# Kernel tuning notes

Hardware: AMD Instinct MI355X
Metric: run time of the kernel (lower is better)

The kernel has to match this reference:

```python
import jax, jax.numpy as jnp
import numpy as np

B, N, RESC, LAT, UNIT = 8, 32, 256.0, 1536, 512
CHS = [64, 64, 128, 256, 512, 512]
HS = [128, 64, 32, 16, 8, 1]


def _align(feat, P):
    # torch F.grid_sample(feat, 2*P.unsqueeze(-2)/RESC - 1, 'bilinear', 'border', align_corners=False).squeeze(-1)
    # feat: [B,C,H,W], P: [B,M,2] (x,y) pixel coords in [0,RESC); returns [B,C,M]
    Bn, C, H, W = feat.shape
    gx = 2.0 * P[..., 0] / RESC - 1.0
    gy = 2.0 * P[..., 1] / RESC - 1.0
    # align_corners=False unnormalize, then border clamp
    x = jnp.clip(((gx + 1.0) * W - 1.0) * 0.5, 0.0, W - 1.0)
    y = jnp.clip(((gy + 1.0) * H - 1.0) * 0.5, 0.0, H - 1.0)
    x0 = jnp.floor(x); y0 = jnp.floor(y)
    wx = (x - x0)[:, None, :]; wy = (y - y0)[:, None, :]
    x0i = x0.astype(jnp.int32); y0i = y0.astype(jnp.int32)
    x1i = jnp.minimum(x0i + 1, W - 1); y1i = jnp.minimum(y0i + 1, H - 1)
    flat = feat.reshape(Bn, C, H * W)
    def gat(yi, xi):
        return jnp.take_along_axis(flat, (yi * W + xi)[:, None, :], axis=2)  # [B,C,M]
    v00 = gat(y0i, x0i); v01 = gat(y0i, x1i); v10 = gat(y1i, x0i); v11 = gat(y1i, x1i)
    return v00 * (1 - wx) * (1 - wy) + v01 * wx * (1 - wy) + v10 * (1 - wx) * wy + v11 * wx * wy


def _conv1(x, w, b):
    # 1x1 Conv1d: [B,Cin,M] x [Cout,Cin] -> [B,Cout,M]
    return jnp.einsum('bci,oc->boi', x, w) + b[None, :, None]


def _rescls(x, p):
    # ResCls(n=1): intro -> (relu(BN) -> chorus, residual) -> outro ; BN in eval mode
    iw, ib, bg, bb, bm, bv, cw, cb, ow, ob = p
    x = _conv1(x, iw, ib)
    d = jax.nn.relu((x - bm[None, :, None]) * (bg / jnp.sqrt(bv + 1e-5))[None, :, None] + bb[None, :, None])
    x = x + _conv1(d, cw, cb)
    return _conv1(x, ow, ob)


def _forward(feats, P, n, gp, pp):
    # node features: concat of per-level aligned features  [B, LAT, N]
    F_ = jnp.concatenate([_align(f, P) for f in feats], axis=1)
    # edge midpoints ep[b, i*N+j] = (P[i] + P[j]) / 2  -> [B, N*N, 2]
    ep = ((P[:, :, None, :] + P[:, None, :, :]) * 0.5).reshape(B, N * N, 2)
    # L: first LAT channels = F[:, :, i], next LAT channels = F[:, :, j]
    Fi = jnp.broadcast_to(F_[:, :, :, None], (B, LAT, N, N)).reshape(B, LAT, N * N)
    Fj = jnp.broadcast_to(F_[:, :, None, :], (B, LAT, N, N)).reshape(B, LAT, N * N)
    E = jnp.concatenate([_align(f, ep) for f in feats], axis=1)  # [B, LAT, N*N]
    CE = jnp.concatenate([Fi, Fj, E], axis=1)  # [B, 3*LAT, N*N]
    gate = jax.nn.sigmoid(_rescls(CE, gp))  # [B, 1, N*N]
    pr = _rescls(CE, pp)  # [B, 64, N*N]
    pr = pr / jnp.maximum(jnp.linalg.norm(pr, axis=1, keepdims=True), 1e-12)  # F.normalize(dim=1)
    m = jnp.arange(N) < n[:, None]  # [B, N]
    mask = (m[:, None, :] & m[:, :, None]).reshape(B, 1, N * N).astype(CE.dtype)
    return (gate * pr * mask).reshape(B, 64, N, N)


def setup_inputs() -> dict:
    key = jax.random.key(0)
    ks = jax.random.split(key, 20)
    d = {}
    for i, (c, h) in enumerate(zip(CHS, HS)):
        d[f'feat{i}'] = jax.random.normal(ks[i], (B, c, h, h), jnp.float32)
    d['P'] = jax.random.uniform(ks[6], (B, N, 2), jnp.float32) * RESC
    d['n'] = jax.random.randint(ks[7], (B,), 16, N + 1, jnp.int32)
    def w(k, shape):
        return jax.random.normal(k, shape, jnp.float32) * 0.02
    for pre, cout, k0 in (('g', 1, 8), ('p', 64, 12)):
        d[pre + '_iw'] = w(ks[k0], (UNIT, 3 * LAT)); d[pre + '_ib'] = jnp.zeros((UNIT,), jnp.float32)
        d[pre + '_bg'] = jnp.ones((UNIT,), jnp.float32); d[pre + '_bb'] = jnp.zeros((UNIT,), jnp.float32)
        d[pre + '_bm'] = jnp.zeros((UNIT,), jnp.float32)
        d[pre + '_bv'] = jax.random.uniform(ks[k0 + 1], (UNIT,), jnp.float32) + 0.5
        d[pre + '_cw'] = w(ks[k0 + 2], (UNIT, UNIT)); d[pre + '_cb'] = jnp.zeros((UNIT,), jnp.float32)
        d[pre + '_ow'] = w(ks[k0 + 3], (cout, UNIT)); d[pre + '_ob'] = jnp.zeros((cout,), jnp.float32)
    return d


def reference(feat0, feat1, feat2, feat3, feat4, feat5, P, n,
              g_iw, g_ib, g_bg, g_bb, g_bm, g_bv, g_cw, g_cb, g_ow, g_ob,
              p_iw, p_ib, p_bg, p_bb, p_bm, p_bv, p_cw, p_cb, p_ow, p_ob):
    feats = (feat0, feat1, feat2, feat3, feat4, feat5)
    gp = (g_iw, g_ib, g_bg, g_bb, g_bm, g_bv, g_cw, g_cb, g_ow, g_ob)
    pp = (p_iw, p_ib, p_bg, p_bb, p_bm, p_bv, p_cw, p_cb, p_ow, p_ob)
    return _forward(feats, P, n, gp, pp)
```

## Files before the change

kernel.cpp:

```cpp
#include <hip/hip_runtime.h>
#include <hip/hip_bf16.h>

using bf16 = __hip_bfloat16;
using short8 = __attribute__((ext_vector_type(8))) short;
using f32x4  = __attribute__((ext_vector_type(4))) float;
typedef unsigned int u32;

#define LAT_ 1536

__device__ __forceinline__ void glds16(const bf16* g, bf16* l) {
  __builtin_amdgcn_global_load_lds(
      (const __attribute__((address_space(1))) void*)g,
      (__attribute__((address_space(3))) void*)l, 16, 0, 0);
}

__global__ __launch_bounds__(256) void conv1536_k(const float* __restrict__ g_iw,
                                                  const float* __restrict__ p_iw,
                                                  bf16* __restrict__ Wp) {
  int seg = blockIdx.y;
  int idx = blockIdx.x * 256 + threadIdx.x;
  if (idx >= 512 * 1536) return;
  int r = idx / 1536, c = idx % 1536;
  const float* src; int co;
  switch (seg) {
    case 0: src = g_iw; co = 0;    break;
    case 1: src = g_iw; co = 1536; break;
    case 2: src = p_iw; co = 0;    break;
    case 3: src = p_iw; co = 1536; break;
    case 4: src = g_iw; co = 3072; break;
    default: src = p_iw; co = 3072; break;
  }
  Wp[(long)seg * 512 * 1536 + idx] = __float2bfloat16(src[(long)r * 4608 + co + c]);
}

__global__ __launch_bounds__(256) void conv512_k(const float* __restrict__ g_cw,
                                                 const float* __restrict__ p_cw,
                                                 const float* __restrict__ p_ow,
                                                 const float* __restrict__ f5,
                                                 bf16* __restrict__ dst) {
  int seg = blockIdx.y;
  int idx = blockIdx.x * 256 + threadIdx.x;
  int lim = (seg < 2) ? 262144 : (seg == 2 ? 32768 : 4096);
  if (idx >= lim) return;
  const float* s = seg == 0 ? g_cw : (seg == 1 ? p_cw : (seg == 2 ? p_ow : f5));
  long off = seg == 0 ? 0 : (seg == 1 ? 262144 : (seg == 2 ? 524288 : 557056));
  dst[off + idx] = __float2bfloat16(s[idx]);
}

__global__ void bnconst2_k(const float* g_bg, const float* g_bb, const float* g_bm, const float* g_bv,
                           const float* p_bg, const float* p_bb, const float* p_bm, const float* p_bv,
                           const float* g_ib, const float* p_ib, const float* g_cb, const float* p_cb,
                           float* bn) {
  int k = blockIdx.x * 256 + threadIdx.x;
  if (k >= 512) return;
  float sg = g_bg[k] / sqrtf(g_bv[k] + 1e-5f);
  bn[k] = sg; bn[512 + k] = g_bb[k] - g_bm[k] * sg;
  float sp = p_bg[k] / sqrtf(p_bv[k] + 1e-5f);
  bn[1024 + k] = sp; bn[1536 + k] = p_bb[k] - p_bm[k] * sp;
  bn[2048 + k] = g_ib[k]; bn[2560 + k] = p_ib[k];
  bn[3072 + k] = g_cb[k]; bn[3584 + k] = p_cb[k];
}

template<int C, int W>
__global__ __launch_bounds__(256) void transpose_k(const float* __restrict__ src,
                                                   bf16* __restrict__ dst) {
  constexpr int HW = W * W;
  int b = blockIdx.z;
  int hw0 = blockIdx.x * 64, c0 = blockIdx.y * 64;
  __shared__ bf16 tile[64][72];
  int t = threadIdx.x;
  {
    int cl = t >> 2, h0 = (t & 3) * 16;
    const float* sp = src + (long)(b * C + c0 + cl) * HW + hw0 + h0;
    #pragma unroll
    for (int k = 0; k < 16; k += 4) {
      float4 v = *(const float4*)(sp + k);
      tile[h0 + k + 0][cl] = __float2bfloat16(v.x);
      tile[h0 + k + 1][cl] = __float2bfloat16(v.y);
      tile[h0 + k + 2][cl] = __float2bfloat16(v.z);
      tile[h0 + k + 3][cl] = __float2bfloat16(v.w);
    }
  }
  __syncthreads();
  {
    int hwl = t >> 2, cc = (t & 3) * 16;
    bf16* dp = dst + ((long)b * HW + hw0 + hwl) * C + c0 + cc;
    #pragma unroll
    for (int k = 0; k < 16; k += 2) {
      __hip_bfloat162 pr;
      pr.x = tile[hwl][cc + k];
      pr.y = tile[hwl][cc + k + 1];
      *(__hip_bfloat162*)(dp + k) = pr;
    }
  }
}

__device__ __forceinline__ float blo(u32 r) { return __uint_as_float(r << 16); }
__device__ __forceinline__ float bhi(u32 r) { return __uint_as_float(r & 0xffff0000u); }

template<int C, int W>
__device__ __forceinline__ void proc2(const bf16* __restrict__ T, int b,
    const float* MX, const float* MY, bf16* __restrict__ Sb, int koff, int t) {
  constexpr int C2 = C / 2, HW = W * W;
  const bf16* Tb = T + (long)b * HW * C;
  for (int idx = t; idx < 16 * C2; idx += 256) {
    int q = idx / C2, c2 = idx % C2;
    float x = MX[q], y = MY[q];
    float fx = fminf(fmaxf(x * ((float)W / 256.f) - 0.5f, 0.f), (float)(W - 1));
    float fy = fminf(fmaxf(y * ((float)W / 256.f) - 0.5f, 0.f), (float)(W - 1));
    float x0f = floorf(fx), y0f = floorf(fy);
    float wx = fx - x0f, wy = fy - y0f;
    int x0 = (int)x0f, y0 = (int)y0f;
    int x1 = min(x0 + 1, W - 1), y1 = min(y0 + 1, W - 1);
    u32 r00 = *(const u32*)&Tb[(y0 * W + x0) * C + 2 * c2];
    u32 r01 = *(const u32*)&Tb[(y0 * W + x1) * C + 2 * c2];
    u32 r10 = *(const u32*)&Tb[(y1 * W + x0) * C + 2 * c2];
    u32 r11 = *(const u32*)&Tb[(y1 * W + x1) * C + 2 * c2];
    float w00 = (1.f - wx) * (1.f - wy), w01 = wx * (1.f - wy);
    float w10 = (1.f - wx) * wy,        w11 = wx * wy;
    float vlo = blo(r00) * w00 + blo(r01) * w01 + blo(r10) * w10 + blo(r11) * w11;
    float vhi = bhi(r00) * w00 + bhi(r01) * w01 + bhi(r10) * w10 + bhi(r11) * w11;
    __hip_bfloat162 pr;
    pr.x = __float2bfloat16(vlo);
    pr.y = __float2bfloat16(vhi);
    *(__hip_bfloat162*)&Sb[(long)q * LAT_ + koff + 2 * c2] = pr;
  }
}

__global__ __launch_bounds__(256) void sample3_k(
    const bf16* __restrict__ T0, const bf16* __restrict__ T1, const bf16* __restrict__ T2,
    const bf16* __restrict__ T3, const bf16* __restrict__ T4, const bf16* __restrict__ T5,
    const float* __restrict__ P, bf16* __restrict__ Sball) {
  int b = blockIdx.y, p0 = blockIdx.x * 16, t = threadIdx.x;
  __shared__ float Px[32], Py[32], MX[16], MY[16];
  if (t < 32) { Px[t] = P[(b * 32 + t) * 2]; Py[t] = P[(b * 32 + t) * 2 + 1]; }
  __syncthreads();
  if (t < 16) {
    int m = p0 + t;
    float x, y;
    if (m < 32) { x = Px[m]; y = Py[m]; }
    else { int ij = m - 32, i = ij >> 5, j = ij & 31;
           x = 0.5f * (Px[i] + Px[j]); y = 0.5f * (Py[i] + Py[j]); }
    MX[t] = x; MY[t] = y;
  }
  __syncthreads();
  bf16* Sb = Sball + ((long)b * 1056 + p0) * LAT_;
  proc2<64, 128>(T0, b, MX, MY, Sb, 0,    t);
  proc2<64, 64 >(T1, b, MX, MY, Sb, 64,   t);
  proc2<128, 32>(T2, b, MX, MY, Sb, 128,  t);
  proc2<256, 16>(T3, b, MX, MY, Sb, 256,  t);
  proc2<512, 8 >(T4, b, MX, MY, Sb, 512,  t);
  for (int idx = t; idx < 16 * 256; idx += 256) {
    int q = idx >> 8, c2 = idx & 255;
    *(__hip_bfloat162*)&Sb[(long)q * LAT_ + 1024 + 2 * c2] =
        *(const __hip_bfloat162*)&T5[b * 512 + 2 * c2];
  }
}

__global__ __launch_bounds__(256) void nodegemm_k(
    const bf16* __restrict__ Sball, const bf16* __restrict__ Wp, float* __restrict__ A4) {
  int b = blockIdx.y;
  int n0 = blockIdx.x * 64;
  int t = threadIdx.x, w = t >> 6, lane = t & 63;
  int nn = n0 + w * 16;
  int frow = lane & 15, fko = (lane >> 4) * 8;
  const bf16* Ab = Sball + (long)b * 1056 * LAT_;
  f32x4 acc[2] = {};
  for (int kb = 0; kb < LAT_; kb += 32) {
    short8 bq = *(const short8*)&Wp[(long)(nn + frow) * LAT_ + kb + fko];
    #pragma unroll
    for (int i = 0; i < 2; ++i) {
      short8 aq = *(const short8*)&Ab[(long)(i * 16 + frow) * LAT_ + kb + fko];
      acc[i] = __builtin_amdgcn_mfma_f32_16x16x32_bf16(aq, bq, acc[i], 0, 0, 0);
    }
  }
  #pragma unroll
  for (int i = 0; i < 2; ++i)
    #pragma unroll
    for (int r = 0; r < 4; ++r) {
      int m = i * 16 + (lane >> 4) * 4 + r;
      int n = nn + (lane & 15);
      A4[(long)b * 65536 + m * 2048 + n] = acc[i][r];
    }
}

template<int MODE>
__global__ __launch_bounds__(256) void mgemmB_k(
    const bf16* __restrict__ Abase, const bf16* __restrict__ B0, const bf16* __restrict__ B1,
    const float* __restrict__ bnp, const float* __restrict__ A4,
    bf16* __restrict__ XFh, bf16* __restrict__ DH,
    float* __restrict__ YgF, bf16* __restrict__ Yp16) {
  int m0 = blockIdx.x * 128;
  int n0 = blockIdx.y * 128;
  int b, net = 0, lda, K, ldb;
  const bf16 *A, *Bw;
  if (MODE == 0) {
    b = blockIdx.z;
    A = Abase + (long)b * 1056 * LAT_ + 32 * LAT_; lda = LAT_; K = LAT_;
    Bw = B0; ldb = LAT_;
  } else {
    int z = blockIdx.z; b = z >> 1; net = z & 1;
    A = Abase + (long)b * 1024 * 1024 + net * 512; lda = 1024; K = 512;
    Bw = net ? B1 : B0; ldb = 512;
  }
  __shared__ bf16 Ash[128 * 32];
  __shared__ bf16 Bsh[128 * 32];
  int t = threadIdx.x, w = t >> 6, lane = t & 63;
  int mh = (w & 1) * 64, nh = (w >> 1) * 64;
  int frow = lane & 15, fko = (lane >> 4) * 8;
  int lrow = lane >> 2, lko = (lane & 3) * 8;
  f32x4 acc[4][4] = {};
  for (int kb = 0; kb < K; kb += 32) {
    #pragma unroll
    for (int q = 0; q < 2; ++q) {
      int ra = q * 64 + w * 16 + lrow;
      glds16(&A[(long)(m0 + ra) * lda + kb + lko],  &Ash[ra * 32 + lko]);
      glds16(&Bw[(long)(n0 + ra) * ldb + kb + lko], &Bsh[ra * 32 + lko]);
    }
    __syncthreads();
    short8 af[4], bq[4];
    #pragma unroll
    for (int i = 0; i < 4; ++i) af[i] = *(const short8*)&Ash[(mh + i * 16 + frow) * 32 + fko];
    #pragma unroll
    for (int j = 0; j < 4; ++j) bq[j] = *(const short8*)&Bsh[(nh + j * 16 + frow) * 32 + fko];
    #pragma unroll
    for (int i = 0; i < 4; ++i)
      #pragma unroll
      for (int j = 0; j < 4; ++j)
        acc[i][j] = __builtin_amdgcn_mfma_f32_16x16x32_bf16(af[i], bq[j], acc[i][j], 0, 0, 0);
    __syncthreads();
  }
  #pragma unroll
  for (int i = 0; i < 4; ++i) {
    #pragma unroll
    for (int j = 0; j < 4; ++j) {
      #pragma unroll
      for (int r = 0; r < 4; ++r) {
        int m = m0 + mh + i * 16 + (lane >> 4) * 4 + r;
        int n = n0 + nh + j * 16 + (lane & 15);
        float v = acc[i][j][r];
        if (MODE == 0) {
          int nt = n >> 9, nn2 = n & 511;
          v += bnp[2048 + n]
             + A4[((long)b * 32 + (m >> 5)) * 2048 + nt * 1024 + nn2]
             + A4[((long)b * 32 + (m & 31)) * 2048 + nt * 1024 + 512 + nn2];
          XFh[((long)b * 1024 + m) * 1024 + n] = __float2bfloat16(v);
          float d = fmaxf(fmaf(v, bnp[nt * 1024 + nn2], bnp[nt * 1024 + 512 + nn2]), 0.f);
          DH[((long)b * 1024 + m) * 1024 + n] = __float2bfloat16(d);
        } else {
          v += bnp[3072 + net * 512 + n]
             + __bfloat162float(XFh[((long)b * 1024 + m) * 1024 + net * 512 + n]);
          if (net) Yp16[((long)b * 1024 + m) * 512 + n] = __float2bfloat16(v);
          else     YgF[((long)b * 1024 + m) * 512 + n] = v;
        }
      }
    }
  }
}

__global__ __launch_bounds__(256) void outro_k(
    const bf16* __restrict__ A, const bf16* __restrict__ Bw,
    const float* __restrict__ bias, float* __restrict__ PR) {
  int b = blockIdx.z;
  const bf16* Ab = A + (long)b * 1024 * 512;
  int m0 = blockIdx.x * 128;
  __shared__ bf16 Ash[128][40];
  __shared__ bf16 Bsh[64][40];
  int t = threadIdx.x, w = t >> 6, lane = t & 63;
  int mq = w * 32;
  int frow = lane & 15, fko = (lane >> 4) * 8;
  f32x4 acc[2][4] = {};
  for (int kb = 0; kb < 512; kb += 32) {
    #pragma unroll
    for (int q = 0; q < 2; ++q) {
      int flat = q * 256 + t;
      int r = flat >> 2, ko = (flat & 3) * 8;
      *(uint4*)&Ash[r][ko] = *(const uint4*)&Ab[(long)(m0 + r) * 512 + kb + ko];
    }
    { int r = t >> 2, ko = (t & 3) * 8;
      *(uint4*)&Bsh[r][ko] = *(const uint4*)&Bw[(long)r * 512 + kb + ko]; }
    __syncthreads();
    short8 af[2], bq[4];
    #pragma unroll
    for (int i = 0; i < 2; ++i) af[i] = *(const short8*)&Ash[mq + i * 16 + frow][fko];
    #pragma unroll
    for (int j = 0; j < 4; ++j) bq[j] = *(const short8*)&Bsh[j * 16 + frow][fko];
    #pragma unroll
    for (int i = 0; i < 2; ++i)
      #pragma unroll
      for (int j = 0; j < 4; ++j)
        acc[i][j] = __builtin_amdgcn_mfma_f32_16x16x32_bf16(af[i], bq[j], acc[i][j], 0, 0, 0);
    __syncthreads();
  }
  #pragma unroll
  for (int i = 0; i < 2; ++i)
    #pragma unroll
    for (int j = 0; j < 4; ++j)
      #pragma unroll
      for (int r = 0; r < 4; ++r) {
        int m = m0 + mq + i * 16 + (lane >> 4) * 4 + r;
        int n = j * 16 + (lane & 15);
        PR[((long)b * 1024 + m) * 64 + n] = acc[i][j][r] + bias[n];
      }
}

__global__ __launch_bounds__(256) void final2_k(
    const float* __restrict__ Yg, const float* __restrict__ PR,
    const float* __restrict__ g_ow, const float* __restrict__ g_ob,
    const int* __restrict__ n, float* __restrict__ out) {
  int gw = blockIdx.x * 4 + (threadIdx.x >> 6);
  int lane = threadIdx.x & 63;
  int b = gw >> 10, ij = gw & 1023;
  const float* yrow = Yg + ((long)b * 1024 + ij) * 512;
  float g = 0.f;
  #pragma unroll
  for (int q = 0; q < 8; ++q) { int o = q * 64 + lane; g = fmaf(g_ow[o], yrow[o], g); }
  #pragma unroll
  for (int off = 32; off; off >>= 1) g += __shfl_down(g, off);
  g = __shfl(g, 0) + g_ob[0];
  float gate = 1.f / (1.f + expf(-g));
  int i = ij >> 5, j = ij & 31, nb = n[b];
  float maskv = (i < nb && j < nb) ? 1.f : 0.f;
  float v = PR[((long)b * 1024 + ij) * 64 + lane];
  float ss = v * v;
  #pragma unroll
  for (int off = 32; off; off >>= 1) ss += __shfl_down(ss, off);
  ss = __shfl(ss, 0);
  float scale = gate * maskv / fmaxf(sqrtf(ss), 1e-12f);
  out[((long)b * 64 + lane) * 1024 + ij] = v * scale;
}

extern "C" void kernel_launch(void* const* d_in, const int* in_sizes, int n_in,
                              void* d_out, int out_size, void* d_ws, size_t ws_size,
                              hipStream_t stream) {
  const float* f0 = (const float*)d_in[0];
  const float* f1 = (const float*)d_in[1];
  const float* f2 = (const float*)d_in[2];
  const float* f3 = (const float*)d_in[3];
  const float* f4 = (const float*)d_in[4];
  const float* f5 = (const float*)d_in[5];
  const float* P  = (const float*)d_in[6];
  const int*   n  = (const int*)d_in[7];
  const float *g_iw=(const float*)d_in[8],  *g_ib=(const float*)d_in[9],
              *g_bg=(const float*)d_in[10], *g_bb=(const float*)d_in[11],
              *g_bm=(const float*)d_in[12], *g_bv=(const float*)d_in[13],
              *g_cw=(const float*)d_in[14], *g_cb=(const float*)d_in[15],
              *g_ow=(const float*)d_in[16], *g_ob=(const float*)d_in[17];
  const float *p_iw=(const float*)d_in[18], *p_ib=(const float*)d_in[19],
              *p_bg=(const float*)d_in[20], *p_bb=(const float*)d_in[21],
              *p_bm=(const float*)d_in[22], *p_bv=(const float*)d_in[23],
              *p_cw=(const float*)d_in[24], *p_cb=(const float*)d_in[25],
              *p_ow=(const float*)d_in[26], *p_ob=(const float*)d_in[27];
  float* out = (float*)d_out;
  char* wsb = (char*)d_ws;

  bf16*  Sb   = (bf16*)(wsb + 0);
  bf16*  Wp   = (bf16*)(wsb + 25952256);
  bf16*  CWp  = (bf16*)(wsb + 35389440);
  float* bnp  = (float*)(wsb + 36511744);
  float* A4   = (float*)(wsb + 36528128);
  bf16*  XFh  = (bf16*)(wsb + 38625280);
  bf16*  DH   = (bf16*)(wsb + 55402496);
  bf16*  Yp16 = (bf16*)(wsb + 72179712);
  bf16*  T0 = (bf16*)(wsb + 38625280);
  bf16*  T1 = (bf16*)(wsb + 55402496);
  bf16*  T2 = (bf16*)(wsb + 59596800);
  bf16*  T3 = (bf16*)(wsb + 61693952);
  bf16*  T4 = (bf16*)(wsb + 62742528);
  float* YgF = (float*)(wsb + 0);
  float* PR  = (float*)(wsb + 36528128);

  bf16* gcw16 = CWp;
  bf16* pcw16 = CWp + 262144;
  bf16* pow16 = CWp + 524288;
  bf16* T5    = CWp + 557056;
  bf16* WpE   = Wp + (long)2048 * LAT_;

  conv1536_k<<<dim3(3072, 6), 256, 0, stream>>>(g_iw, p_iw, Wp);
  conv512_k<<<dim3(1024, 4), 256, 0, stream>>>(g_cw, p_cw, p_ow, f5, CWp);
  bnconst2_k<<<dim3(2), 256, 0, stream>>>(g_bg, g_bb, g_bm, g_bv, p_bg, p_bb, p_bm, p_bv,
                                          g_ib, p_ib, g_cb, p_cb, bnp);
  transpose_k<64, 128><<<dim3(256, 1, 8), 256, 0, stream>>>(f0, T0);
  transpose_k<64, 64 ><<<dim3(64, 1, 8),  256, 0, stream>>>(f1, T1);
  transpose_k<128, 32><<<dim3(16, 2, 8),  256, 0, stream>>>(f2, T2);
  transpose_k<256, 16><<<dim3(4, 4, 8),   256, 0, stream>>>(f3, T3);
  transpose_k<512, 8 ><<<dim3(1, 8, 8),   256, 0, stream>>>(f4, T4);

  sample3_k<<<dim3(66, 8), 256, 0, stream>>>(T0, T1, T2, T3, T4, T5, P, Sb);
  nodegemm_k<<<dim3(32, 8), 256, 0, stream>>>(Sb, Wp, A4);

  mgemmB_k<0><<<dim3(8, 8, 8), 256, 0, stream>>>(Sb, WpE, nullptr, bnp, A4,
                                                 XFh, DH, nullptr, nullptr);
  mgemmB_k<1><<<dim3(8, 4, 16), 256, 0, stream>>>(DH, gcw16, pcw16, bnp, nullptr,
                                                  XFh, nullptr, YgF, Yp16);
  outro_k<<<dim3(8, 1, 8), 256, 0, stream>>>(Yp16, pow16, p_ob, PR);
  final2_k<<<dim3(2048), 256, 0, stream>>>(YgF, PR, g_ow, g_ob, n, out);
}
```

Baseline: 296.4 us.

## Exploit edge symmetry, fold gate-net chorus into a vector, merge small kernels

Edge midpoints are symmetric in (i,j), so only the 528 upper-triangle pairs are sampled and pushed through the edge GEMM, and results are scattered to both (i,j) and (j,i). The gate network's chorus GEMM and 1-channel outro are folded algebraically into a precomputed vector u = g_ow·g_cw, so the gate becomes a dot product over XF and DH rows in the final kernel. Transposes and the small weight-packing kernels are merged into single launches, LDS loads gain an XOR swizzle, and the outro tiling is halved. The edge epilogue now does scattered paired writes plus extra A4 loads, which costs some coalescing.

```diff
diff --git a/kernel.cpp b/kernel.cpp
--- a/kernel.cpp
+++ b/kernel.cpp
@@ -13,10 +13,12 @@
       (const __attribute__((address_space(1))) void*)g,
       (__attribute__((address_space(3))) void*)l, 16, 0, 0);
 }
-
-__global__ __launch_bounds__(256) void conv1536_k(const float* __restrict__ g_iw,
-                                                  const float* __restrict__ p_iw,
-                                                  bf16* __restrict__ Wp) {
+__device__ __forceinline__ float b2f(bf16 x) { return __bfloat162float(x); }
+__device__ __forceinline__ bf16 f2b(float x) { return __float2bfloat16(x); }
+
+__global__ __launch_bounds__(256) void packA_k(const float* __restrict__ g_iw,
+                                               const float* __restrict__ p_iw,
+                                               bf16* __restrict__ Wp) {
   int seg = blockIdx.y;
   int idx = blockIdx.x * 256 + threadIdx.x;
   if (idx >= 512 * 1536) return;
@@ -30,55 +32,64 @@
     case 4: src = g_iw; co = 3072; break;
     default: src = p_iw; co = 3072; break;
   }
-  Wp[(long)seg * 512 * 1536 + idx] = __float2bfloat16(src[(long)r * 4608 + co + c]);
-}
-
-__global__ __launch_bounds__(256) void conv512_k(const float* __restrict__ g_cw,
-                                                 const float* __restrict__ p_cw,
-                                                 const float* __restrict__ p_ow,
-                                                 const float* __restrict__ f5,
-                                                 bf16* __restrict__ dst) {
-  int seg = blockIdx.y;
+  Wp[(long)seg * 512 * 1536 + idx] = f2b(src[(long)r * 4608 + co + c]);
+}
+
+__global__ __launch_bounds__(256) void packB_k(
+    const float* __restrict__ p_cw, const float* __restrict__ p_ow, const float* __restrict__ f5,
+    const float* __restrict__ g_bg, const float* __restrict__ g_bb, const float* __restrict__ g_bm,
+    const float* __restrict__ g_bv, const float* __restrict__ p_bg, const float* __restrict__ p_bb,
+    const float* __restrict__ p_bm, const float* __restrict__ p_bv,
+    const float* __restrict__ g_ib, const float* __restrict__ p_ib, const float* __restrict__ p_cb,
+    const float* __restrict__ g_ow, const float* __restrict__ g_cw,
+    bf16* __restrict__ pcw16, bf16* __restrict__ pow16, bf16* __restrict__ T5,
+    float* __restrict__ bnp, int* __restrict__ PAIR, float* __restrict__ u) {
   int idx = blockIdx.x * 256 + threadIdx.x;
-  int lim = (seg < 2) ? 262144 : (seg == 2 ? 32768 : 4096);
-  if (idx >= lim) return;
-  const float* s = seg == 0 ? g_cw : (seg == 1 ? p_cw : (seg == 2 ? p_ow : f5));
-  long off = seg == 0 ? 0 : (seg == 1 ? 262144 : (seg == 2 ? 524288 : 557056));
-  dst[off + idx] = __float2bfloat16(s[idx]);
-}
-
-__global__ void bnconst2_k(const float* g_bg, const float* g_bb, const float* g_bm, const float* g_bv,
-                           const float* p_bg, const float* p_bb, const float* p_bm, const float* p_bv,
-                           const float* g_ib, const float* p_ib, const float* g_cb, const float* p_cb,
-                           float* bn) {
-  int k = blockIdx.x * 256 + threadIdx.x;
-  if (k >= 512) return;
-  float sg = g_bg[k] / sqrtf(g_bv[k] + 1e-5f);
-  bn[k] = sg; bn[512 + k] = g_bb[k] - g_bm[k] * sg;
-  float sp = p_bg[k] / sqrtf(p_bv[k] + 1e-5f);
-  bn[1024 + k] = sp; bn[1536 + k] = p_bb[k] - p_bm[k] * sp;
-  bn[2048 + k] = g_ib[k]; bn[2560 + k] = p_ib[k];
-  bn[3072 + k] = g_cb[k]; bn[3584 + k] = p_cb[k];
+  if (blockIdx.y == 0) {
+    if (idx < 262144) pcw16[idx] = f2b(p_cw[idx]);
+    return;
+  }
+  if (idx < 32768) { pow16[idx] = f2b(p_ow[idx]); return; }
+  if (idx < 36864) { int e = idx - 32768; T5[e] = f2b(f5[e]); return; }
+  if (idx < 37376) {
+    int k = idx - 36864;
+    float sg = g_bg[k] / sqrtf(g_bv[k] + 1e-5f);
+    bnp[k] = sg; bnp[512 + k] = g_bb[k] - g_bm[k] * sg;
+    float sp = p_bg[k] / sqrtf(p_bv[k] + 1e-5f);
+    bnp[1024 + k] = sp; bnp[1536 + k] = p_bb[k] - p_bm[k] * sp;
+    bnp[2048 + k] = g_ib[k]; bnp[2560 + k] = p_ib[k];
+    bnp[3584 + k] = p_cb[k];
+    return;
+  }
+  if (idx < 37904) {
+    int t = idx - 37376;
+    int i = 0, rem = t;
+    while (rem >= 32 - i) { rem -= 32 - i; ++i; }
+    PAIR[t] = i * 32 + (i + rem);
+    return;
+  }
+  if (idx < 38416) {
+    int k = idx - 37904;
+    float s = 0.f;
+    for (int n = 0; n < 512; ++n) s = fmaf(g_ow[n], g_cw[n * 512 + k], s);
+    u[k] = s;
+  }
 }
 
 template<int C, int W>
-__global__ __launch_bounds__(256) void transpose_k(const float* __restrict__ src,
-                                                   bf16* __restrict__ dst) {
+__device__ __forceinline__ void trans_tile(const float* __restrict__ src, bf16* __restrict__ dst,
+                                           int b, int hw0, int c0, bf16 (*tile)[72], int t) {
   constexpr int HW = W * W;
-  int b = blockIdx.z;
-  int hw0 = blockIdx.x * 64, c0 = blockIdx.y * 64;
-  __shared__ bf16 tile[64][72];
-  int t = threadIdx.x;
   {
     int cl = t >> 2, h0 = (t & 3) * 16;
     const float* sp = src + (long)(b * C + c0 + cl) * HW + hw0 + h0;
     #pragma unroll
     for (int k = 0; k < 16; k += 4) {
       float4 v = *(const float4*)(sp + k);
-      tile[h0 + k + 0][cl] = __float2bfloat16(v.x);
-      tile[h0 + k + 1][cl] = __float2bfloat16(v.y);
-      tile[h0 + k + 2][cl] = __float2bfloat16(v.z);
-      tile[h0 + k + 3][cl] = __float2bfloat16(v.w);
+      tile[h0 + k + 0][cl] = f2b(v.x);
+      tile[h0 + k + 1][cl] = f2b(v.y);
+      tile[h0 + k + 2][cl] = f2b(v.z);
+      tile[h0 + k + 3][cl] = f2b(v.w);
     }
   }
   __syncthreads();
@@ -93,6 +104,20 @@
       *(__hip_bfloat162*)(dp + k) = pr;
     }
   }
+}
+
+__global__ __launch_bounds__(256) void transpose_all_k(
+    const float* __restrict__ f0, const float* __restrict__ f1, const float* __restrict__ f2,
+    const float* __restrict__ f3, const float* __restrict__ f4,
+    bf16* __restrict__ T0, bf16* __restrict__ T1, bf16* __restrict__ T2,
+    bf16* __restrict__ T3, bf16* __restrict__ T4) {
+  __shared__ bf16 tile[64][72];
+  int b = blockIdx.y, tt = blockIdx.x, t = threadIdx.x;
+  if (tt < 256)      trans_tile<64, 128>(f0, T0, b, tt * 64, 0, tile, t);
+  else if (tt < 320) trans_tile<64, 64 >(f1, T1, b, (tt - 256) * 64, 0, tile, t);
+  else if (tt < 352) { int q = tt - 320; trans_tile<128, 32>(f2, T2, b, (q & 15) * 64, (q >> 4) * 64, tile, t); }
+  else if (tt < 368) { int q = tt - 352; trans_tile<256, 16>(f3, T3, b, (q & 3) * 64, (q >> 2) * 64, tile, t); }
+  else               { int q = tt - 368; trans_tile<512, 8 >(f4, T4, b, 0, q * 64, tile, t); }
 }
 
 __device__ __forceinline__ float blo(u32 r) { return __uint_as_float(r << 16); }
@@ -121,16 +146,15 @@
     float vlo = blo(r00) * w00 + blo(r01) * w01 + blo(r10) * w10 + blo(r11) * w11;
     float vhi = bhi(r00) * w00 + bhi(r01) * w01 + bhi(r10) * w10 + bhi(r11) * w11;
     __hip_bfloat162 pr;
-    pr.x = __float2bfloat16(vlo);
-    pr.y = __float2bfloat16(vhi);
+    pr.x = f2b(vlo); pr.y = f2b(vhi);
     *(__hip_bfloat162*)&Sb[(long)q * LAT_ + koff + 2 * c2] = pr;
   }
 }
 
-__global__ __launch_bounds__(256) void sample3_k(
+__global__ __launch_bounds__(256) void sample4_k(
     const bf16* __restrict__ T0, const bf16* __restrict__ T1, const bf16* __restrict__ T2,
     const bf16* __restrict__ T3, const bf16* __restrict__ T4, const bf16* __restrict__ T5,
-    const float* __restrict__ P, bf16* __restrict__ Sball) {
+    const float* __restrict__ P, const int* __restrict__ PAIR, bf16* __restrict__ Sball) {
   int b = blockIdx.y, p0 = blockIdx.x * 16, t = threadIdx.x;
   __shared__ float Px[32], Py[32], MX[16], MY[16];
   if (t < 32) { Px[t] = P[(b * 32 + t) * 2]; Py[t] = P[(b * 32 + t) * 2 + 1]; }
@@ -139,12 +163,12 @@
     int m = p0 + t;
     float x, y;
     if (m < 32) { x = Px[m]; y = Py[m]; }
-    else { int ij = m - 32, i = ij >> 5, j = ij & 31;
+    else { int pr_ = PAIR[m - 32]; int i = pr_ >> 5, j = pr_ & 31;
            x = 0.5f * (Px[i] + Px[j]); y = 0.5f * (Py[i] + Py[j]); }
     MX[t] = x; MY[t] = y;
   }
   __syncthreads();
-  bf16* Sb = Sball + ((long)b * 1056 + p0) * LAT_;
+  bf16* Sb = Sball + ((long)b * 560 + p0) * LAT_;
   proc2<64, 128>(T0, b, MX, MY, Sb, 0,    t);
   proc2<64, 64 >(T1, b, MX, MY, Sb, 64,   t);
   proc2<128, 32>(T2, b, MX, MY, Sb, 128,  t);
@@ -164,7 +188,7 @@
   int t = threadIdx.x, w = t >> 6, lane = t & 63;
   int nn = n0 + w * 16;
   int frow = lane & 15, fko = (lane >> 4) * 8;
-  const bf16* Ab = Sball + (long)b * 1056 * LAT_;
+  const bf16* Ab = Sball + (long)b * 560 * LAT_;
   f32x4 acc[2] = {};
   for (int kb = 0; kb < LAT_; kb += 32) {
     short8 bq = *(const short8*)&Wp[(long)(nn + frow) * LAT_ + kb + fko];
@@ -184,45 +208,37 @@
     }
 }
 
-template<int MODE>
-__global__ __launch_bounds__(256) void mgemmB_k(
-    const bf16* __restrict__ Abase, const bf16* __restrict__ B0, const bf16* __restrict__ B1,
+__global__ __launch_bounds__(256) void edge_k(
+    const bf16* __restrict__ Sball, const bf16* __restrict__ WpE,
     const float* __restrict__ bnp, const float* __restrict__ A4,
-    bf16* __restrict__ XFh, bf16* __restrict__ DH,
-    float* __restrict__ YgF, bf16* __restrict__ Yp16) {
-  int m0 = blockIdx.x * 128;
-  int n0 = blockIdx.y * 128;
-  int b, net = 0, lda, K, ldb;
-  const bf16 *A, *Bw;
-  if (MODE == 0) {
-    b = blockIdx.z;
-    A = Abase + (long)b * 1056 * LAT_ + 32 * LAT_; lda = LAT_; K = LAT_;
-    Bw = B0; ldb = LAT_;
-  } else {
-    int z = blockIdx.z; b = z >> 1; net = z & 1;
-    A = Abase + (long)b * 1024 * 1024 + net * 512; lda = 1024; K = 512;
-    Bw = net ? B1 : B0; ldb = 512;
-  }
+    const int* __restrict__ PAIR,
+    bf16* __restrict__ XFh, bf16* __restrict__ DH) {
+  int b = blockIdx.z;
+  int m0 = blockIdx.x * 128, n0 = blockIdx.y * 128;
+  const bf16* A = Sball + (long)b * 560 * LAT_ + 32 * LAT_;
   __shared__ bf16 Ash[128 * 32];
   __shared__ bf16 Bsh[128 * 32];
   int t = threadIdx.x, w = t >> 6, lane = t & 63;
   int mh = (w & 1) * 64, nh = (w >> 1) * 64;
-  int frow = lane & 15, fko = (lane >> 4) * 8;
-  int lrow = lane >> 2, lko = (lane & 3) * 8;
+  int frow = lane & 15, cf = lane >> 4;
+  int lrow = lane >> 2, lchunk = lane & 3;
+  int csw = (lrow >> 1) & 3;
+  int sA = (cf ^ ((frow >> 1) & 3)) * 8;
   f32x4 acc[4][4] = {};
-  for (int kb = 0; kb < K; kb += 32) {
+  for (int kb = 0; kb < LAT_; kb += 32) {
     #pragma unroll
     for (int q = 0; q < 2; ++q) {
       int ra = q * 64 + w * 16 + lrow;
-      glds16(&A[(long)(m0 + ra) * lda + kb + lko],  &Ash[ra * 32 + lko]);
-      glds16(&Bw[(long)(n0 + ra) * ldb + kb + lko], &Bsh[ra * 32 + lko]);
+      int am = min(m0 + ra, 527);
+      glds16(&A[(long)am * LAT_ + kb + (lchunk ^ csw) * 8],        &Ash[ra * 32 + lchunk * 8]);
+      glds16(&WpE[(long)(n0 + ra) * LAT_ + kb + (lchunk ^ csw) * 8], &Bsh[ra * 32 + lchunk * 8]);
     }
     __syncthreads();
     short8 af[4], bq[4];
     #pragma unroll
-    for (int i = 0; i < 4; ++i) af[i] = *(const short8*)&Ash[(mh + i * 16 + frow) * 32 + fko];
-    #pragma unroll
-    for (int j = 0; j < 4; ++j) bq[j] = *(const short8*)&Bsh[(nh + j * 16 + frow) * 32 + fko];
+    for (int i = 0; i < 4; ++i) af[i] = *(const short8*)&Ash[(mh + i * 16 + frow) * 32 + sA];
+    #pragma unroll
+    for (int j = 0; j < 4; ++j) bq[j] = *(const short8*)&Bsh[(nh + j * 16 + frow) * 32 + sA];
     #pragma unroll
     for (int i = 0; i < 4; ++i)
       #pragma unroll
@@ -233,92 +249,143 @@
   #pragma unroll
   for (int i = 0; i < 4; ++i) {
     #pragma unroll
-    for (int j = 0; j < 4; ++j) {
+    for (int r = 0; r < 4; ++r) {
+      int mu = m0 + mh + i * 16 + (lane >> 4) * 4 + r;
+      if (mu >= 528) continue;
+      int pr_ = PAIR[mu];
+      int ii = pr_ >> 5, jj = pr_ & 31;
+      #pragma unroll
+      for (int j = 0; j < 4; ++j) {
+        int n = n0 + nh + j * 16 + (lane & 15);
+        int nt = n >> 9, nn2 = n & 511;
+        float base = acc[i][j][r] + bnp[2048 + n];
+        float sc = bnp[nt * 1024 + nn2], sh = bnp[nt * 1024 + 512 + nn2];
+        float Ai_i = A4[((long)b * 32 + ii) * 2048 + nt * 1024 + nn2];
+        float Aj_j = A4[((long)b * 32 + jj) * 2048 + nt * 1024 + 512 + nn2];
+        long e1 = ((long)b * 1024 + ii * 32 + jj) * 1024 + n;
+        float v1 = base + Ai_i + Aj_j;
+        XFh[e1] = f2b(v1);
+        DH[e1]  = f2b(fmaxf(fmaf(v1, sc, sh), 0.f));
+        if (ii != jj) {
+          float Ai_j = A4[((long)b * 32 + jj) * 2048 + nt * 1024 + nn2];
+          float Aj_i = A4[((long)b * 32 + ii) * 2048 + nt * 1024 + 512 + nn2];
+          long e2 = ((long)b * 1024 + jj * 32 + ii) * 1024 + n;
+          float v2 = base + Ai_j + Aj_i;
+          XFh[e2] = f2b(v2);
+          DH[e2]  = f2b(fmaxf(fmaf(v2, sc, sh), 0.f));
+        }
+      }
+    }
+  }
+}
+
+__global__ __launch_bounds__(256) void chorus_k(
+    const bf16* __restrict__ DH, const bf16* __restrict__ pcw16,
+    const float* __restrict__ bnp, const bf16* __restrict__ XFh,
+    bf16* __restrict__ Yp16) {
+  int b = blockIdx.z;
+  int m0 = blockIdx.x * 128, n0 = blockIdx.y * 128;
+  const bf16* A = DH + (long)b * 1024 * 1024 + 512;
+  __shared__ bf16 Ash[128 * 32];
+  __shared__ bf16 Bsh[128 * 32];
+  int t = threadIdx.x, w = t >> 6, lane = t & 63;
+  int mh = (w & 1) * 64, nh = (w >> 1) * 64;
+  int frow = lane & 15, cf = lane >> 4;
+  int lrow = lane >> 2, lchunk = lane & 3;
+  int csw = (lrow >> 1) & 3;
+  int sA = (cf ^ ((frow >> 1) & 3)) * 8;
+  f32x4 acc[4][4] = {};
+  for (int kb = 0; kb < 512; kb += 32) {
+    #pragma unroll
+    for (int q = 0; q < 2; ++q) {
+      int ra = q * 64 + w * 16 + lrow;
+      glds16(&A[(long)(m0 + ra) * 1024 + kb + (lchunk ^ csw) * 8],     &Ash[ra * 32 + lchunk * 8]);
+      glds16(&pcw16[(long)(n0 + ra) * 512 + kb + (lchunk ^ csw) * 8],  &Bsh[ra * 32 + lchunk * 8]);
+    }
+    __syncthreads();
+    short8 af[4], bq[4];
+    #pragma unroll
+    for (int i = 0; i < 4; ++i) af[i] = *(const short8*)&Ash[(mh + i * 16 + frow) * 32 + sA];
+    #pragma unroll
+    for (int j = 0; j < 4; ++j) bq[j] = *(const short8*)&Bsh[(nh + j * 16 + frow) * 32 + sA];
+    #pragma unroll
+    for (int i = 0; i < 4; ++i)
+      #pragma unroll
+      for (int j = 0; j < 4; ++j)
+        acc[i][j] = __builtin_amdgcn_mfma_f32_16x16x32_bf16(af[i], bq[j], acc[i][j], 0, 0, 0);
+    __syncthreads();
+  }
+  #pragma unroll
+  for (int i = 0; i < 4; ++i)
+    #pragma unroll
+    for (int j = 0; j < 4; ++j)
       #pragma unroll
       for (int r = 0; r < 4; ++r) {
         int m = m0 + mh + i * 16 + (lane >> 4) * 4 + r;
         int n = n0 + nh + j * 16 + (lane & 15);
-        float v = acc[i][j][r];
-        if (MODE == 0) {
-          int nt = n >> 9, nn2 = n & 511;
-          v += bnp[2048 + n]
-             + A4[((long)b * 32 + (m >> 5)) * 2048 + nt * 1024 + nn2]
-             + A4[((long)b * 32 + (m & 31)) * 2048 + nt * 1024 + 512 + nn2];
-          XFh[((long)b * 1024 + m) * 1024 + n] = __float2bfloat16(v);
-          float d = fmaxf(fmaf(v, bnp[nt * 1024 + nn2], bnp[nt * 1024 + 512 + nn2]), 0.f);
-          DH[((long)b * 1024 + m) * 1024 + n] = __float2bfloat16(d);
-        } else {
-          v += bnp[3072 + net * 512 + n]
-             + __bfloat162float(XFh[((long)b * 1024 + m) * 1024 + net * 512 + n]);
-          if (net) Yp16[((long)b * 1024 + m) * 512 + n] = __float2bfloat16(v);
-          else     YgF[((long)b * 1024 + m) * 512 + n] = v;
-        }
+        float v = acc[i][j][r] + bnp[3584 + n]
+                + b2f(XFh[((long)b * 1024 + m) * 1024 + 512 + n]);
+        Yp16[((long)b * 1024 + m) * 512 + n] = f2b(v);
       }
-    }
-  }
 }
 
 __global__ __launch_bounds__(256) void outro_k(
-    const bf16* __restrict__ A, const bf16* __restrict__ Bw,
-    const float* __restrict__ bias, float* __restrict__ PR) {
+    const bf16* __restrict__ Yp16, const bf16* __restrict__ pow16,
+    const float* __restrict__ p_ob, float* __restrict__ PR) {
   int b = blockIdx.z;
-  const bf16* Ab = A + (long)b * 1024 * 512;
-  int m0 = blockIdx.x * 128;
-  __shared__ bf16 Ash[128][40];
+  const bf16* Ab = Yp16 + (long)b * 1024 * 512;
+  int m0 = blockIdx.x * 64;
+  __shared__ bf16 Ash[64][40];
   __shared__ bf16 Bsh[64][40];
   int t = threadIdx.x, w = t >> 6, lane = t & 63;
-  int mq = w * 32;
+  int mq = w * 16;
   int frow = lane & 15, fko = (lane >> 4) * 8;
-  f32x4 acc[2][4] = {};
+  f32x4 acc[4] = {};
   for (int kb = 0; kb < 512; kb += 32) {
-    #pragma unroll
-    for (int q = 0; q < 2; ++q) {
-      int flat = q * 256 + t;
-      int r = flat >> 2, ko = (flat & 3) * 8;
+    { int r = t >> 2, ko = (t & 3) * 8;
       *(uint4*)&Ash[r][ko] = *(const uint4*)&Ab[(long)(m0 + r) * 512 + kb + ko];
-    }
-    { int r = t >> 2, ko = (t & 3) * 8;
-      *(uint4*)&Bsh[r][ko] = *(const uint4*)&Bw[(long)r * 512 + kb + ko]; }
-    __syncthreads();
-    short8 af[2], bq[4];
-    #pragma unroll
-    for (int i = 0; i < 2; ++i) af[i] = *(const short8*)&Ash[mq + i * 16 + frow][fko];
-    #pragma unroll
-    for (int j = 0; j < 4; ++j) bq[j] = *(const short8*)&Bsh[j * 16 + frow][fko];
-    #pragma unroll
-    for (int i = 0; i < 2; ++i)
-      #pragma unroll
-      for (int j = 0; j < 4; ++j)
-        acc[i][j] = __builtin_amdgcn_mfma_f32_16x16x32_bf16(af[i], bq[j], acc[i][j], 0, 0, 0);
-    __syncthreads();
-  }
-  #pragma unroll
-  for (int i = 0; i < 2; ++i)
-    #pragma unroll
-    for (int j = 0; j < 4; ++j)
-      #pragma unroll
-      for (int r = 0; r < 4; ++r) {
-        int m = m0 + mq + i * 16 + (lane >> 4) * 4 + r;
-        int n = j * 16 + (lane & 15);
-        PR[((long)b * 1024 + m) * 64 + n] = acc[i][j][r] + bias[n];
-      }
-}
-
-__global__ __launch_bounds__(256) void final2_k(
-    const float* __restrict__ Yg, const float* __restrict__ PR,
-    const float* __restrict__ g_ow, const float* __restrict__ g_ob,
+      *(uint4*)&Bsh[r][ko] = *(const uint4*)&pow16[(long)r * 512 + kb + ko]; }
+    __syncthreads();
+    short8 af = *(const short8*)&Ash[mq + frow][fko];
+    #pragma unroll
+    for (int j = 0; j < 4; ++j) {
+      short8 bq = *(const short8*)&Bsh[j * 16 + frow][fko];
+      acc[j] = __builtin_amdgcn_mfma_f32_16x16x32_bf16(af, bq, acc[j], 0, 0, 0);
+    }
+    __syncthreads();
+  }
+  #pragma unroll
+  for (int j = 0; j < 4; ++j)
+    #pragma unroll
+    for (int r = 0; r < 4; ++r) {
+      int m = m0 + mq + (lane >> 4) * 4 + r;
+      int n = j * 16 + (lane & 15);
+      PR[((long)b * 1024 + m) * 64 + n] = acc[j][r] + p_ob[n];
+    }
+}
+
+__global__ __launch_bounds__(256) void final3_k(
+    const bf16* __restrict__ XFh, const bf16* __restrict__ DH, const float* __restrict__ PR,
+    const float* __restrict__ u, const float* __restrict__ g_ow,
+    const float* __restrict__ g_cb, const float* __restrict__ g_ob,
     const int* __restrict__ n, float* __restrict__ out) {
   int gw = blockIdx.x * 4 + (threadIdx.x >> 6);
   int lane = threadIdx.x & 63;
   int b = gw >> 10, ij = gw & 1023;
-  const float* yrow = Yg + ((long)b * 1024 + ij) * 512;
-  float g = 0.f;
-  #pragma unroll
-  for (int q = 0; q < 8; ++q) { int o = q * 64 + lane; g = fmaf(g_ow[o], yrow[o], g); }
-  #pragma unroll
-  for (int off = 32; off; off >>= 1) g += __shfl_down(g, off);
-  g = __shfl(g, 0) + g_ob[0];
-  float gate = 1.f / (1.f + expf(-g));
+  const bf16* xr = XFh + ((long)b * 1024 + ij) * 1024;
+  const bf16* dr = DH  + ((long)b * 1024 + ij) * 1024;
+  float gl = 0.f;
+  #pragma unroll
+  for (int q = 0; q < 8; ++q) {
+    int nn = q * 64 + lane;
+    float go = g_ow[nn];
+    gl = fmaf(go, b2f(xr[nn]) + g_cb[nn], gl);
+    gl = fmaf(u[nn], b2f(dr[nn]), gl);
+  }
+  #pragma unroll
+  for (int off = 32; off; off >>= 1) gl += __shfl_down(gl, off);
+  gl = __shfl(gl, 0) + g_ob[0];
+  float gate = 1.f / (1.f + expf(-gl));
   int i = ij >> 5, j = ij & 31, nb = n[b];
   float maskv = (i < nb && j < nb) ? 1.f : 0.f;
   float v = PR[((long)b * 1024 + ij) * 64 + lane];
@@ -354,45 +421,35 @@
   float* out = (float*)d_out;
   char* wsb = (char*)d_ws;
 
-  bf16*  Sb   = (bf16*)(wsb + 0);
-  bf16*  Wp   = (bf16*)(wsb + 25952256);
-  bf16*  CWp  = (bf16*)(wsb + 35389440);
-  float* bnp  = (float*)(wsb + 36511744);
-  float* A4   = (float*)(wsb + 36528128);
-  bf16*  XFh  = (bf16*)(wsb + 38625280);
-  bf16*  DH   = (bf16*)(wsb + 55402496);
-  bf16*  Yp16 = (bf16*)(wsb + 72179712);
-  bf16*  T0 = (bf16*)(wsb + 38625280);
-  bf16*  T1 = (bf16*)(wsb + 55402496);
-  bf16*  T2 = (bf16*)(wsb + 59596800);
-  bf16*  T3 = (bf16*)(wsb + 61693952);
-  bf16*  T4 = (bf16*)(wsb + 62742528);
-  float* YgF = (float*)(wsb + 0);
-  float* PR  = (float*)(wsb + 36528128);
-
-  bf16* gcw16 = CWp;
-  bf16* pcw16 = CWp + 262144;
-  bf16* pow16 = CWp + 524288;
-  bf16* T5    = CWp + 557056;
-  bf16* WpE   = Wp + (long)2048 * LAT_;
-
-  conv1536_k<<<dim3(3072, 6), 256, 0, stream>>>(g_iw, p_iw, Wp);
-  conv512_k<<<dim3(1024, 4), 256, 0, stream>>>(g_cw, p_cw, p_ow, f5, CWp);
-  bnconst2_k<<<dim3(2), 256, 0, stream>>>(g_bg, g_bb, g_bm, g_bv, p_bg, p_bb, p_bm, p_bv,
-                                          g_ib, p_ib, g_cb, p_cb, bnp);
-  transpose_k<64, 128><<<dim3(256, 1, 8), 256, 0, stream>>>(f0, T0);
-  transpose_k<64, 64 ><<<dim3(64, 1, 8),  256, 0, stream>>>(f1, T1);
-  transpose_k<128, 32><<<dim3(16, 2, 8),  256, 0, stream>>>(f2, T2);
-  transpose_k<256, 16><<<dim3(4, 4, 8),   256, 0, stream>>>(f3, T3);
-  transpose_k<512, 8 ><<<dim3(1, 8, 8),   256, 0, stream>>>(f4, T4);
-
-  sample3_k<<<dim3(66, 8), 256, 0, stream>>>(T0, T1, T2, T3, T4, T5, P, Sb);
+  bf16*  Sb    = (bf16*)(wsb + 0);
+  bf16*  Wp    = (bf16*)(wsb + 13762560);
+  bf16*  pcw16 = (bf16*)(wsb + 23199744);
+  bf16*  pow16 = (bf16*)(wsb + 23724032);
+  bf16*  T5    = (bf16*)(wsb + 23789568);
+  float* bnp   = (float*)(wsb + 23797760);
+  int*   PAIR  = (int*)(wsb + 23814144);
+  float* u     = (float*)(wsb + 23816256);
+  float* A4    = (float*)(wsb + 23818304);
+  bf16*  XFh   = (bf16*)(wsb + 25915456);
+  bf16*  DH    = (bf16*)(wsb + 42692672);
+  bf16*  Yp16  = (bf16*)(wsb + 59469888);
+  float* PR    = (float*)(wsb + 67858496);
+  bf16*  T0 = (bf16*)(wsb + 25915456);
+  bf16*  T1 = (bf16*)(wsb + 42692672);
+  bf16*  T2 = (bf16*)(wsb + 46886976);
+  bf16*  T3 = (bf16*)(wsb + 48984128);
+  bf16*  T4 = (bf16*)(wsb + 50032704);
+  bf16*  WpE = Wp + (long)2048 * LAT_;
+
+  packA_k<<<dim3(3072, 6), 256, 0, stream>>>(g_iw, p_iw, Wp);
+  packB_k<<<dim3(1024, 2), 256, 0, stream>>>(p_cw, p_ow, f5,
+      g_bg, g_bb, g_bm, g_bv, p_bg, p_bb, p_bm, p_bv, g_ib, p_ib, p_cb,
+      g_ow, g_cw, pcw16, pow16, T5, bnp, PAIR, u);
+  transpose_all_k<<<dim3(376, 8), 256, 0, stream>>>(f0, f1, f2, f3, f4, T0, T1, T2, T3, T4);
+  sample4_k<<<dim3(35, 8), 256, 0, stream>>>(T0, T1, T2, T3, T4, T5, P, PAIR, Sb);
   nodegemm_k<<<dim3(32, 8), 256, 0, stream>>>(Sb, Wp, A4);
-
-  mgemmB_k<0><<<dim3(8, 8, 8), 256, 0, stream>>>(Sb, WpE, nullptr, bnp, A4,
-                                                 XFh, DH, nullptr, nullptr);
-  mgemmB_k<1><<<dim3(8, 4, 16), 256, 0, stream>>>(DH, gcw16, pcw16, bnp, nullptr,
-                                                  XFh, nullptr, YgF, Yp16);
-  outro_k<<<dim3(8, 1, 8), 256, 0, stream>>>(Yp16, pow16, p_ob, PR);
-  final2_k<<<dim3(2048), 256, 0, stream>>>(YgF, PR, g_ow, g_ob, n, out);
-}
+  edge_k<<<dim3(5, 8, 8), 256, 0, stream>>>(Sb, WpE, bnp, A4, PAIR, XFh, DH);
+  chorus_k<<<dim3(8, 4, 8), 256, 0, stream>>>(DH, pcw16, bnp, XFh, Yp16);
+  outro_k<<<dim3(16, 1, 8), 256, 0, stream>>>(Yp16, pow16, p_ob, PR);
+  final3_k<<<dim3(2048), 256, 0, stream>>>(XFh, DH, PR, u, g_ow, g_cb, g_ob, n, out);
+}
```

Result: slower. 337.3 us (+13.8%).
